# Optimization experiments

Hardware: AMD Instinct MI355X
Metric: run time of the kernel (lower is better)

## Reference

```python
import jax, jax.numpy as jnp
import numpy as np

SEQ_LEN = 2048
NUM_GLOBAL = 32
NEG_INF = float('-inf')


def _build_mask(seq_len=SEQ_LEN, num_global=NUM_GLOBAL):
    # Causal mask: triu(ones).T == lower-triangular ones; zeros -> -inf, ones -> 0.
    m = np.where(np.tril(np.ones((seq_len, seq_len), dtype=np.float32)) == 1.0, 0.0, NEG_INF)
    # Deterministic 'random.sample' of global tokens (fixed for reproducibility).
    rng = np.random.default_rng(0)
    gtok = rng.choice(seq_len, size=num_global, replace=False)
    m[:, gtok] = 0.0
    m[gtok, :] = 0.0
    return jnp.asarray(m)


def setup_inputs() -> dict:
    key = jax.random.key(0)
    ks = jax.random.split(key, 9)
    B, S, D_IN, D_QK = 8, SEQ_LEN, 1024, 128
    return {
        'q': jax.random.normal(ks[0], (B, S, D_IN), dtype=jnp.float32),
        'k': jax.random.normal(ks[1], (B, S, D_IN), dtype=jnp.float32),
        'v': jax.random.normal(ks[2], (B, S, D_IN), dtype=jnp.float32),
        'Wq': jax.random.normal(ks[3], (D_QK, D_IN), dtype=jnp.float32) * 0.02,
        'bq': jax.random.normal(ks[4], (D_QK,), dtype=jnp.float32) * 0.02,
        'Wk': jax.random.normal(ks[5], (D_QK, D_IN), dtype=jnp.float32) * 0.02,
        'bk': jax.random.normal(ks[6], (D_QK,), dtype=jnp.float32) * 0.02,
        'Wv': jax.random.normal(ks[7], (D_QK, D_IN), dtype=jnp.float32) * 0.02,
        'bv': jax.random.normal(ks[8], (D_QK,), dtype=jnp.float32) * 0.02,
    }


def reference(q, k, v, Wq, bq, Wk, bk, Wv, bv):
    # Linear projections (torch nn.Linear: x @ W.T + b)
    Q = jnp.einsum('bsd,qd->bsq', q, Wq) + bq   # [B,S,dq]
    K = jnp.einsum('bsd,qd->bsq', k, Wk) + bk   # [B,S,dk]
    V = jnp.einsum('bsd,qd->bsq', v, Wv) + bv   # [B,S,dk]
    mask = _build_mask()                        # [S,S] static causal+global
    scale = K.shape[-1] ** 0.5
    scores = jnp.einsum('bqd,bkd->bqk', Q, K)   # dense QK^T [B,S,S]
    scores = (scores + mask) / scale            # (-inf stays -inf)
    attn = jax.nn.softmax(scores, axis=-1)
    return jnp.einsum('bqk,bkd->bqd', attn, V)
```

## Files before the change

kernel.cpp:

```cpp
#include <hip/hip_runtime.h>
#include <cstdint>

constexpr int SEQ  = 2048;
constexpr int DIN  = 1024;
constexpr int DQK  = 128;
constexpr int NB   = 8;
constexpr int MTOT = NB * SEQ;
constexpr float INV_SCALE = 0.08838834764831845f;

typedef __attribute__((ext_vector_type(8))) short  short8;
typedef __attribute__((ext_vector_type(4))) float  floatx4;
typedef __attribute__((ext_vector_type(4))) int    intx4;

struct GM { unsigned long long w[32]; };

static void compute_gtok(unsigned long long bits[32]) {
  typedef unsigned __int128 u128;
  uint32_t pool[4];
  uint32_t hc = 0x43b0d7e5u;
  auto hashmix = [&hc](uint32_t v) -> uint32_t {
    v ^= hc; hc *= 0x931e8875u; v *= hc; v ^= v >> 16; return v;
  };
  auto mixf = [](uint32_t x, uint32_t y) -> uint32_t {
    uint32_t r = x * 0xca01f9ddu - y * 0x4973f715u;
    r ^= r >> 16; return r;
  };
  pool[0] = hashmix(0u);
  for (int i = 1; i < 4; ++i) pool[i] = hashmix(0u);
  for (int s = 0; s < 4; ++s)
    for (int d = 0; d < 4; ++d)
      if (s != d) pool[d] = mixf(pool[d], hashmix(pool[s]));
  uint32_t hb = 0x8b51f9ddu;
  uint32_t st[8];
  for (int i = 0; i < 8; ++i) {
    uint32_t dv = pool[i & 3];
    dv ^= hb; hb *= 0x58f38dedu; dv *= hb; dv ^= dv >> 16;
    st[i] = dv;
  }
  uint64_t sv[4];
  for (int i = 0; i < 4; ++i)
    sv[i] = (uint64_t)st[2 * i] | ((uint64_t)st[2 * i + 1] << 32);
  const u128 MUL = ((u128)2549297995355413924ULL << 64) | (u128)4865540595714422341ULL;
  u128 initstate = ((u128)sv[0] << 64) | sv[1];
  u128 initseq   = ((u128)sv[2] << 64) | sv[3];
  u128 state = 0;
  u128 inc = (initseq << 1) | 1;
  state = state * MUL + inc;
  state += initstate;
  state = state * MUL + inc;
  bool has32 = false; uint32_t cache32 = 0;
  auto next64 = [&]() -> uint64_t {
    state = state * MUL + inc;
    uint64_t hi = (uint64_t)(state >> 64);
    uint64_t lo = (uint64_t)state;
    unsigned rot = (unsigned)(state >> 122);
    uint64_t x = hi ^ lo;
    return (x >> rot) | (x << ((64u - rot) & 63u));
  };
  auto next32 = [&]() -> uint32_t {
    if (has32) { has32 = false; return cache32; }
    uint64_t n = next64();
    has32 = true; cache32 = (uint32_t)(n >> 32);
    return (uint32_t)n;
  };
  bool in_set[SEQ];
  for (int i = 0; i < SEQ; ++i) in_set[i] = false;
  for (uint32_t j = 2016; j < 2048; ++j) {
    uint32_t rng_excl = j + 1;
    uint64_t m = (uint64_t)next32() * rng_excl;
    uint32_t leftover = (uint32_t)m;
    if (leftover < rng_excl) {
      uint32_t threshold = (0xFFFFFFFFu - j) % rng_excl;
      while (leftover < threshold) {
        m = (uint64_t)next32() * rng_excl;
        leftover = (uint32_t)m;
      }
    }
    uint32_t val = (uint32_t)(m >> 32);
    if (in_set[val]) in_set[j] = true;
    else in_set[val] = true;
  }
  for (int i = 0; i < 32; ++i) bits[i] = 0ULL;
  for (int t = 0; t < SEQ; ++t)
    if (in_set[t]) bits[t >> 6] |= (1ULL << (t & 63));
}

__device__ __forceinline__ void ldsld16(const void* g, void* l) {
  __builtin_amdgcn_global_load_lds(
      (const __attribute__((address_space(1))) unsigned int*)g,
      (__attribute__((address_space(3))) unsigned int*)l, 16, 0, 0);
}
__device__ __forceinline__ bool gbit(const GM& g, int j) {
  return (g.w[j >> 6] >> (j & 63)) & 1ULL;
}
__device__ __forceinline__ void split4(float4 x, unsigned hw[2], unsigned lw[2]) {
  unsigned u0 = __float_as_uint(x.x), u1 = __float_as_uint(x.y);
  unsigned u2 = __float_as_uint(x.z), u3 = __float_as_uint(x.w);
  hw[0] = __builtin_amdgcn_perm(u1, u0, 0x07060302u);
  hw[1] = __builtin_amdgcn_perm(u3, u2, 0x07060302u);
  unsigned r0 = __float_as_uint(x.x - __uint_as_float(u0 & 0xFFFF0000u));
  unsigned r1 = __float_as_uint(x.y - __uint_as_float(u1 & 0xFFFF0000u));
  unsigned r2 = __float_as_uint(x.z - __uint_as_float(u2 & 0xFFFF0000u));
  unsigned r3 = __float_as_uint(x.w - __uint_as_float(u3 & 0xFFFF0000u));
  lw[0] = __builtin_amdgcn_perm(r1, r0, 0x07060302u);
  lw[1] = __builtin_amdgcn_perm(r3, r2, 0x07060302u);
}
__device__ __forceinline__ void split1(float v, unsigned short& h, unsigned short& l) {
  unsigned u = __float_as_uint(v);
  h = (unsigned short)(u >> 16);
  float rr = v - __uint_as_float(u & 0xFFFF0000u);
  l = (unsigned short)(__float_as_uint(rr) >> 16);
}
__device__ __forceinline__ unsigned short bfr_rne(float v) {
  unsigned u = __float_as_uint(v);
  return (unsigned short)((u + 0x7FFFu + ((u >> 16) & 1u)) >> 16);
}

__global__ __launch_bounds__(256) void wconv_kernel(
    const float* __restrict__ Wq, const float* __restrict__ Wk, const float* __restrict__ Wv,
    unsigned short* __restrict__ Whi, unsigned short* __restrict__ Wlo) {
  const float* W = blockIdx.y == 0 ? Wq : blockIdx.y == 1 ? Wk : Wv;
  size_t base = (size_t)blockIdx.y * DQK * DIN;
  int e = (blockIdx.x * 256 + threadIdx.x) * 4;
  float4 x = *(const float4*)&W[e];
  unsigned hw[2], lw[2];
  split4(x, hw, lw);
  *(uint2*)&Whi[base + e] = make_uint2(hw[0], hw[1]);
  *(uint2*)&Wlo[base + e] = make_uint2(lw[0], lw[1]);
}

__global__ __launch_bounds__(256, 3) void proj_kernel(
    const float* __restrict__ xq, const float* __restrict__ xk, const float* __restrict__ xv,
    const unsigned short* __restrict__ Whi, const unsigned short* __restrict__ Wlo,
    const float* __restrict__ bq, const float* __restrict__ bk, const float* __restrict__ bv,
    unsigned short* __restrict__ Qb, unsigned short* __restrict__ Kb,
    unsigned short* __restrict__ Vth) {
  const int which = blockIdx.y;
  const float* X    = which == 0 ? xq : which == 1 ? xk : xv;
  const float* bias = which == 0 ? bq : which == 1 ? bk : bv;
  const int m0 = blockIdx.x * 64;

  __shared__ unsigned short Xh[64 * 64];
  __shared__ unsigned short Xl[64 * 64];
  __shared__ unsigned short Wh[128 * 64];
  __shared__ unsigned short Wl[128 * 64];

  const int tid = threadIdx.x;
  const int w = tid >> 6, lane = tid & 63, l15 = lane & 15, quad = lane >> 4;
  const int mh = (w >> 1) * 32, nh = (w & 1) * 64;

  floatx4 acc[2][4] = {};
  float biasv[4];
#pragma unroll
  for (int j = 0; j < 4; ++j) biasv[j] = bias[nh + j * 16 + l15];

  const unsigned short* WhiP = Whi + (size_t)which * DQK * DIN;
  const unsigned short* WloP = Wlo + (size_t)which * DQK * DIN;

  for (int kb = 0; kb < DIN; kb += 64) {
    __syncthreads();
#pragma unroll
    for (int i = 0; i < 4; ++i) {
      int f = tid + i * 256;
      int r = f >> 4, c4 = f & 15;
      float4 x = *(const float4*)&X[(size_t)(m0 + r) * DIN + kb + c4 * 4];
      unsigned hw[2], lw[2];
      split4(x, hw, lw);
      int off = r * 64 + (((c4 >> 1) ^ (r & 7)) * 8) + (c4 & 1) * 4;
      *(uint2*)&Xh[off] = make_uint2(hw[0], hw[1]);
      *(uint2*)&Xl[off] = make_uint2(lw[0], lw[1]);
    }
#pragma unroll
    for (int i = 0; i < 8; ++i) {
      int c = w * 8 + i;
      int plane = c >> 4, cc = c & 15;
      int F = cc * 1024 + lane * 16;
      int n = F >> 7, gs = (F >> 4) & 7, gl = gs ^ (n & 7);
      const unsigned short* gp = (plane ? WloP : WhiP) + (size_t)n * DIN + kb + gl * 8;
      ldsld16(gp, (char*)(plane ? Wl : Wh) + cc * 1024);
    }
    __syncthreads();
#pragma unroll
    for (int ks = 0; ks < 2; ++ks) {
      short8 Ah[2], Al[2], Bh[4], Bl[4];
#pragma unroll
      for (int ms = 0; ms < 2; ++ms) {
        int off = (mh + ms * 16 + l15) * 64 + (((ks * 4 + quad) ^ (l15 & 7)) * 8);
        Ah[ms] = *(const short8*)&Xh[off];
        Al[ms] = *(const short8*)&Xl[off];
      }
#pragma unroll
      for (int ns = 0; ns < 4; ++ns) {
        int off = (nh + ns * 16 + l15) * 64 + (((ks * 4 + quad) ^ (l15 & 7)) * 8);
        Bh[ns] = *(const short8*)&Wh[off];
        Bl[ns] = *(const short8*)&Wl[off];
      }
#pragma unroll
      for (int i = 0; i < 2; ++i)
#pragma unroll
        for (int j = 0; j < 4; ++j) {
          floatx4 c = acc[i][j];
          c = __builtin_amdgcn_mfma_f32_16x16x32_bf16(Ah[i], Bh[j], c, 0, 0, 0);
          c = __builtin_amdgcn_mfma_f32_16x16x32_bf16(Ah[i], Bl[j], c, 0, 0, 0);
          c = __builtin_amdgcn_mfma_f32_16x16x32_bf16(Al[i], Bh[j], c, 0, 0, 0);
          acc[i][j] = c;
        }
    }
  }

  if (which < 2) {
    unsigned short* O = which == 0 ? Qb : Kb;
#pragma unroll
    for (int i = 0; i < 2; ++i)
#pragma unroll
      for (int j = 0; j < 4; ++j)
#pragma unroll
        for (int r = 0; r < 4; ++r) {
          int m = mh + i * 16 + quad * 4 + r;
          int n = nh + j * 16 + l15;
          O[(size_t)(m0 + m) * DQK + n] = bfr_rne(acc[i][j][r] + biasv[j]);
        }
  } else {
    __syncthreads();
    unsigned short* VH = Wh;
#pragma unroll
    for (int i = 0; i < 2; ++i)
#pragma unroll
      for (int j = 0; j < 4; ++j)
#pragma unroll
        for (int r = 0; r < 4; ++r) {
          int s = mh + i * 16 + quad * 4 + r;
          int d = nh + j * 16 + l15;
          VH[d * 64 + (((s >> 3) ^ (d & 7)) * 8) + (s & 7)] =
              bfr_rne(acc[i][j][r] + biasv[j]);
        }
    __syncthreads();
    int b = m0 >> 11, s0 = m0 & 2047;
#pragma unroll
    for (int i = 0; i < 4; ++i) {
      int cch = i * 256 + tid;
      int d = cch >> 3, gI = cch & 7;
      int loff = d * 64 + ((gI ^ (d & 7)) * 8);
      intx4 vh = *(const intx4*)&VH[loff];
      *(intx4*)&Vth[((size_t)b * DQK + d) * SEQ + s0 + gI * 8] = vh;
    }
  }
}

__global__ __launch_bounds__(256, 3) void attn_kernel(
    const unsigned short* __restrict__ Qb, const unsigned short* __restrict__ Kb,
    const unsigned short* __restrict__ Vth,
    float* __restrict__ Opart, float2* __restrict__ ML, GM g, unsigned int t64) {
  __shared__ unsigned short Ks[64 * 128];
  __shared__ unsigned short Vh[128 * 64];
  __shared__ unsigned short Ph[4][16 * 72];
  __shared__ unsigned short Pl[4][16 * 72];

  const int tid = threadIdx.x;
  const int w = tid >> 6, lane = tid & 63, l15 = lane & 15, quad = lane >> 4;
  const int b = blockIdx.y;
  const int qt = blockIdx.x / 3, s3 = blockIdx.x - qt * 3;
  const int qs = qt * 64;

  short8 qf[4];
  const unsigned short* Qrow = Qb + ((size_t)(b * SEQ + qs + w * 16 + l15)) * DQK;
#pragma unroll
  for (int j = 0; j < 4; ++j) qf[j] = *(const short8*)&Qrow[j * 32 + quad * 8];

  int rowi[4]; bool growb[4];
#pragma unroll
  for (int r = 0; r < 4; ++r) {
    rowi[r] = qs + w * 16 + quad * 4 + r;
    growb[r] = gbit(g, rowi[r]);
  }

  floatx4 o[8] = {};
  float m_r[4] = {-1e30f, -1e30f, -1e30f, -1e30f};
  float l_r[4] = {0.f, 0.f, 0.f, 0.f};

  const bool qhasg = (t64 >> qt) & 1;
  const unsigned short* KbB = Kb  + (size_t)b * SEQ * DQK;
  const unsigned short* VhB = Vth + (size_t)b * DQK * SEQ;

  for (int kt = s3; kt < 32; kt += 3) {
    const int ks0 = kt * 64;
    if (!((ks0 <= qs + 63) || ((t64 >> kt) & 1) || qhasg)) continue;

    __syncthreads();
#pragma unroll
    for (int i = 0; i < 8; ++i) {
      int c = w * 8 + i;
      if (c < 16) {
        int F = c * 1024 + lane * 16;
        int r = F >> 8, gs = (F >> 4) & 15, gl = gs ^ (r & 15);
        ldsld16(KbB + (size_t)(ks0 + r) * DQK + gl * 8, (char*)Ks + c * 1024);
      } else {
        int cc = c - 16;
        int F = cc * 1024 + lane * 16;
        int d = F >> 7, gs = (F >> 4) & 7, gl = gs ^ (d & 7);
        ldsld16(VhB + (size_t)d * SEQ + ks0 + gl * 8, (char*)Vh + cc * 1024);
      }
    }
    __syncthreads();

    floatx4 S[4];
#pragma unroll
    for (int c4 = 0; c4 < 4; ++c4) {
      floatx4 s = {0.f, 0.f, 0.f, 0.f};
#pragma unroll
      for (int j = 0; j < 4; ++j) {
        short8 kf = *(const short8*)&Ks[(c4 * 16 + l15) * 128 + (((j * 4 + quad) ^ l15) * 8)];
        s = __builtin_amdgcn_mfma_f32_16x16x32_bf16(qf[j], kf, s, 0, 0, 0);
      }
      S[c4] = s;
    }

    float z[4][4];
    float mx[4] = {-1e30f, -1e30f, -1e30f, -1e30f};
#pragma unroll
    for (int c4 = 0; c4 < 4; ++c4) {
      int col = ks0 + c4 * 16 + l15;
      bool cg = gbit(g, col);
#pragma unroll
      for (int r = 0; r < 4; ++r) {
        bool ok = (col <= rowi[r]) || cg || growb[r];
        float zz = ok ? S[c4][r] * INV_SCALE : -1e30f;
        z[c4][r] = zz;
        mx[r] = fmaxf(mx[r], zz);
      }
    }
#pragma unroll
    for (int d = 1; d < 16; d <<= 1)
#pragma unroll
      for (int r = 0; r < 4; ++r) mx[r] = fmaxf(mx[r], __shfl_xor(mx[r], d));
    float alpha[4], rs[4] = {0.f, 0.f, 0.f, 0.f};
#pragma unroll
    for (int r = 0; r < 4; ++r) {
      float mn = fmaxf(m_r[r], mx[r]);
      alpha[r] = __expf(m_r[r] - mn);
      m_r[r] = mn;
    }
    float p[4][4];
#pragma unroll
    for (int c4 = 0; c4 < 4; ++c4)
#pragma unroll
      for (int r = 0; r < 4; ++r) {
        float pp = __expf(z[c4][r] - m_r[r]);
        p[c4][r] = pp;
        rs[r] += pp;
      }
#pragma unroll
    for (int d = 1; d < 16; d <<= 1)
#pragma unroll
      for (int r = 0; r < 4; ++r) rs[r] += __shfl_xor(rs[r], d);
#pragma unroll
    for (int r = 0; r < 4; ++r) l_r[r] = l_r[r] * alpha[r] + rs[r];
#pragma unroll
    for (int n = 0; n < 8; ++n)
#pragma unroll
      for (int r = 0; r < 4; ++r) o[n][r] *= alpha[r];

#pragma unroll
    for (int c4 = 0; c4 < 4; ++c4)
#pragma unroll
      for (int r = 0; r < 4; ++r) {
        unsigned short h, lo;
        split1(p[c4][r], h, lo);
        int off = (quad * 4 + r) * 72 + c4 * 16 + l15;
        Ph[w][off] = h; Pl[w][off] = lo;
      }
    short8 pf[2], pg[2];
#pragma unroll
    for (int kq = 0; kq < 2; ++kq) {
      int off = l15 * 72 + kq * 32 + quad * 8;
      pf[kq] = *(const short8*)&Ph[w][off];
      pg[kq] = *(const short8*)&Pl[w][off];
    }

#pragma unroll
    for (int n = 0; n < 8; ++n) {
      int drow = n * 16 + l15;
#pragma unroll
      for (int kq = 0; kq < 2; ++kq) {
        int off = drow * 64 + (((kq * 4 + quad) ^ (drow & 7)) * 8);
        short8 vhf = *(const short8*)&Vh[off];
        floatx4 c = o[n];
        c = __builtin_amdgcn_mfma_f32_16x16x32_bf16(pf[kq], vhf, c, 0, 0, 0);
        c = __builtin_amdgcn_mfma_f32_16x16x32_bf16(pg[kq], vhf, c, 0, 0, 0);
        o[n] = c;
      }
    }
  }

  const size_t grp = (size_t)(b * 32 + qt) * 3 + s3;
  float* Op = Opart + grp * 64 * 128;
#pragma unroll
  for (int n = 0; n < 8; ++n)
#pragma unroll
    for (int r = 0; r < 4; ++r)
      Op[(w * 16 + quad * 4 + r) * 128 + n * 16 + l15] = o[n][r];
  if (l15 == 0) {
#pragma unroll
    for (int r = 0; r < 4; ++r)
      ML[grp * 64 + w * 16 + quad * 4 + r] = make_float2(m_r[r], l_r[r]);
  }
}

__global__ __launch_bounds__(256) void merge_kernel(
    const float* __restrict__ Opart, const float2* __restrict__ ML,
    float* __restrict__ Out) {
  const int t = threadIdx.x;
  const int row = blockIdx.x * 2 + (t >> 7);
  const int col = t & 127;
  const int grp = row >> 6;
  const int rin = row & 63;
  const size_t base = (size_t)grp * 3;
  float2 ml0 = ML[(base + 0) * 64 + rin];
  float2 ml1 = ML[(base + 1) * 64 + rin];
  float2 ml2 = ML[(base + 2) * 64 + rin];
  const float m = fmaxf(fmaxf(ml0.x, ml1.x), ml2.x);
  const float w0 = __expf(ml0.x - m), w1 = __expf(ml1.x - m), w2 = __expf(ml2.x - m);
  const float denom = w0 * ml0.y + w1 * ml1.y + w2 * ml2.y;
  const float o0 = Opart[((base + 0) * 64 + rin) * 128 + col];
  const float o1 = Opart[((base + 1) * 64 + rin) * 128 + col];
  const float o2 = Opart[((base + 2) * 64 + rin) * 128 + col];
  Out[(size_t)row * 128 + col] = (w0 * o0 + w1 * o1 + w2 * o2) / denom;
}

extern "C" void kernel_launch(void* const* d_in, const int* in_sizes, int n_in,
                              void* d_out, int out_size, void* d_ws, size_t ws_size,
                              hipStream_t stream) {
  const float* q  = (const float*)d_in[0];
  const float* k  = (const float*)d_in[1];
  const float* v  = (const float*)d_in[2];
  const float* Wq = (const float*)d_in[3];
  const float* bq = (const float*)d_in[4];
  const float* Wk = (const float*)d_in[5];
  const float* bk = (const float*)d_in[6];
  const float* Wv = (const float*)d_in[7];
  const float* bv = (const float*)d_in[8];
  float* out = (float*)d_out;

  unsigned short* Qb  = (unsigned short*)d_ws;
  unsigned short* Kb2 = Qb  + (size_t)MTOT * DQK;
  unsigned short* Vth = Kb2 + (size_t)MTOT * DQK;
  unsigned short* Whi = Vth + (size_t)MTOT * DQK;
  unsigned short* Wlo = Whi + (size_t)3 * DQK * DIN;
  float*  Opart = (float*)(Wlo + (size_t)3 * DQK * DIN);
  float2* ML    = (float2*)(Opart + (size_t)3 * MTOT * DQK);

  GM g;
  compute_gtok(g.w);
  unsigned int t64 = 0;
  for (int t = 0; t < 32; ++t) if (g.w[t] != 0ULL) t64 |= (1u << t);

  hipLaunchKernelGGL(wconv_kernel, dim3(128, 3), dim3(256), 0, stream,
                     Wq, Wk, Wv, Whi, Wlo);
  hipLaunchKernelGGL(proj_kernel, dim3(256, 3), dim3(256), 0, stream,
                     q, k, v, Whi, Wlo, bq, bk, bv, Qb, Kb2, Vth);
  hipLaunchKernelGGL(attn_kernel, dim3(96, 8), dim3(256), 0, stream,
                     Qb, Kb2, Vth, Opart, ML, g, t64);
  hipLaunchKernelGGL(merge_kernel, dim3(MTOT / 2), dim3(256), 0, stream,
                     Opart, ML, out);
}
```

Baseline: 280.2 us.

## Fuse split-K merge into attention kernel via last-block atomic counter

Removes the separate merge kernel. Each attention block writes its partial output and its max/sum stats, then increments a per-group atomic counter. The third block to finish for a group reads the other two partials and writes the final normalized output, using its own partial straight from registers. The counters are zeroed in the weight-conversion kernel. This saves one kernel launch plus a read and rewrite of one partial, at the cost of fences, an atomic and tail work on the last block.

```diff
diff --git a/kernel.cpp b/kernel.cpp
--- a/kernel.cpp
+++ b/kernel.cpp
@@ -118,7 +118,9 @@
 
 __global__ __launch_bounds__(256) void wconv_kernel(
     const float* __restrict__ Wq, const float* __restrict__ Wk, const float* __restrict__ Wv,
-    unsigned short* __restrict__ Whi, unsigned short* __restrict__ Wlo) {
+    unsigned short* __restrict__ Whi, unsigned short* __restrict__ Wlo,
+    int* __restrict__ Cnt) {
+  if (blockIdx.x == 0 && blockIdx.y == 0) Cnt[threadIdx.x] = 0;
   const float* W = blockIdx.y == 0 ? Wq : blockIdx.y == 1 ? Wk : Wv;
   size_t base = (size_t)blockIdx.y * DQK * DIN;
   int e = (blockIdx.x * 256 + threadIdx.x) * 4;
@@ -250,7 +252,9 @@
 __global__ __launch_bounds__(256, 3) void attn_kernel(
     const unsigned short* __restrict__ Qb, const unsigned short* __restrict__ Kb,
     const unsigned short* __restrict__ Vth,
-    float* __restrict__ Opart, float2* __restrict__ ML, GM g, unsigned int t64) {
+    float* __restrict__ Opart, float2* __restrict__ ML,
+    int* __restrict__ Cnt, float* __restrict__ Out,
+    GM g, unsigned int t64) {
   __shared__ unsigned short Ks[64 * 128];
   __shared__ unsigned short Vh[128 * 64];
   __shared__ unsigned short Ph[4][16 * 72];
@@ -392,7 +396,8 @@
     }
   }
 
-  const size_t grp = (size_t)(b * 32 + qt) * 3 + s3;
+  const int grpI = b * 32 + qt;
+  const size_t grp = (size_t)grpI * 3 + s3;
   float* Op = Opart + grp * 64 * 128;
 #pragma unroll
   for (int n = 0; n < 8; ++n)
@@ -404,27 +409,37 @@
     for (int r = 0; r < 4; ++r)
       ML[grp * 64 + w * 16 + quad * 4 + r] = make_float2(m_r[r], l_r[r]);
   }
-}
-
-__global__ __launch_bounds__(256) void merge_kernel(
-    const float* __restrict__ Opart, const float2* __restrict__ ML,
-    float* __restrict__ Out) {
-  const int t = threadIdx.x;
-  const int row = blockIdx.x * 2 + (t >> 7);
-  const int col = t & 127;
-  const int grp = row >> 6;
-  const int rin = row & 63;
-  const size_t base = (size_t)grp * 3;
-  float2 ml0 = ML[(base + 0) * 64 + rin];
-  float2 ml1 = ML[(base + 1) * 64 + rin];
-  float2 ml2 = ML[(base + 2) * 64 + rin];
-  const float m = fmaxf(fmaxf(ml0.x, ml1.x), ml2.x);
-  const float w0 = __expf(ml0.x - m), w1 = __expf(ml1.x - m), w2 = __expf(ml2.x - m);
-  const float denom = w0 * ml0.y + w1 * ml1.y + w2 * ml2.y;
-  const float o0 = Opart[((base + 0) * 64 + rin) * 128 + col];
-  const float o1 = Opart[((base + 1) * 64 + rin) * 128 + col];
-  const float o2 = Opart[((base + 2) * 64 + rin) * 128 + col];
-  Out[(size_t)row * 128 + col] = (w0 * o0 + w1 * o1 + w2 * o2) / denom;
+
+  __threadfence();
+  __syncthreads();
+  __shared__ int lastFlag;
+  if (tid == 0) lastFlag = (atomicAdd(&Cnt[grpI], 1) == 2);
+  __syncthreads();
+  if (!lastFlag) return;
+  __threadfence();
+
+  const int s3a = s3 + 1 - (s3 + 1 == 3 ? 3 : 0);
+  const int s3b = s3 + 2 - (s3 + 2 >= 3 ? 3 : 0);
+  const float2* MLg = ML + (size_t)grpI * 3 * 64;
+  const float*  OpA = Opart + ((size_t)grpI * 3 + s3a) * 8192;
+  const float*  OpB = Opart + ((size_t)grpI * 3 + s3b) * 8192;
+  float* OutB = Out + ((size_t)b * SEQ + qs) * 128;
+#pragma unroll
+  for (int r = 0; r < 4; ++r) {
+    int rin = w * 16 + quad * 4 + r;
+    float2 mla = MLg[s3a * 64 + rin];
+    float2 mlb = MLg[s3b * 64 + rin];
+    float m = fmaxf(fmaxf(m_r[r], mla.x), mlb.x);
+    float w0 = __expf(m_r[r] - m), wa = __expf(mla.x - m), wb = __expf(mlb.x - m);
+    float rden = 1.0f / (w0 * l_r[r] + wa * mla.y + wb * mlb.y);
+#pragma unroll
+    for (int n = 0; n < 8; ++n) {
+      int c = n * 16 + l15;
+      float oa = OpA[rin * 128 + c];
+      float ob = OpB[rin * 128 + c];
+      OutB[(size_t)rin * 128 + c] = (w0 * o[n][r] + wa * oa + wb * ob) * rden;
+    }
+  }
 }
 
 extern "C" void kernel_launch(void* const* d_in, const int* in_sizes, int n_in,
@@ -448,6 +463,7 @@
   unsigned short* Wlo = Whi + (size_t)3 * DQK * DIN;
   float*  Opart = (float*)(Wlo + (size_t)3 * DQK * DIN);
   float2* ML    = (float2*)(Opart + (size_t)3 * MTOT * DQK);
+  int*    Cnt   = (int*)(ML + (size_t)256 * 3 * 64);
 
   GM g;
   compute_gtok(g.w);
@@ -455,11 +471,9 @@
   for (int t = 0; t < 32; ++t) if (g.w[t] != 0ULL) t64 |= (1u << t);
 
   hipLaunchKernelGGL(wconv_kernel, dim3(128, 3), dim3(256), 0, stream,
-                     Wq, Wk, Wv, Whi, Wlo);
+                     Wq, Wk, Wv, Whi, Wlo, Cnt);
   hipLaunchKernelGGL(proj_kernel, dim3(256, 3), dim3(256), 0, stream,
                      q, k, v, Whi, Wlo, bq, bk, bv, Qb, Kb2, Vth);
   hipLaunchKernelGGL(attn_kernel, dim3(96, 8), dim3(256), 0, stream,
-                     Qb, Kb2, Vth, Opart, ML, g, t64);
-  hipLaunchKernelGGL(merge_kernel, dim3(MTOT / 2), dim3(256), 0, stream,
-                     Opart, ML, out);
-}
+                     Qb, Kb2, Vth, Opart, ML, Cnt, out, g, t64);
+}
```

Result: slower. 428.4 us (+52.9%).
